# Kernel optimization log

Hardware: AMD Instinct MI355X
Metric: run time of the kernel (lower is better)

Reference implementation:

```python
import jax, jax.numpy as jnp
import numpy as np

N_VERTICES = 2000
N_SENSORY = 784
N_EDGES = 500_000
BATCH = 32
T_STEPS = 5
LR_VALUES = 0.1


def setup_inputs() -> dict:
    key = jax.random.key(0)
    k1, k2, k3 = jax.random.split(key, 3)
    values = jax.random.normal(k1, (BATCH, N_VERTICES), dtype=jnp.float32)
    # weight_init 'normal 0.0' -> std = max(0.01, 0) = 0.01 in the torch module
    weights = jax.random.normal(k2, (N_EDGES,), dtype=jnp.float32) * 0.01
    edge_index = jax.random.randint(k3, (2, N_EDGES), 0, N_VERTICES, dtype=jnp.int32)
    # sensory nodes (first 784) are clamped; only internal nodes update
    update_mask = jnp.arange(N_VERTICES) >= N_SENSORY  # bool [N]
    return {
        "values": values,
        "weights": weights,
        "edge_index": edge_index,
        "update_mask": update_mask,
        "T": T_STEPS,
    }


def reference(values, weights, edge_index, update_mask, T):
    """Iterative predictive-coding message passing.

    Each step:
      pred_i  = sum_{e: dst(e)=i} w_e * f(values[src(e)])   (gather-mul-scatter)
      err     = values - pred
      back_j  = sum_{e: src(e)=j} w_e * err[dst(e)]          (reverse scatter)
      dv      = err - f'(values) * back                      (dE/dx)
      values  = values - lr * dv   (sensory nodes clamped)
    """
    src, dst = edge_index[0], edge_index[1]
    n = values.shape[1]
    mask = update_mask[None, :]

    def step(v, _):
        fx = jnp.tanh(v)                                   # [B, N]
        msg = weights[None, :] * fx[:, src]                # [B, E]
        pred = jax.ops.segment_sum(msg.T, dst, num_segments=n).T  # [B, N]
        err = v - pred                                     # [B, N]
        w_err = weights[None, :] * err[:, dst]             # [B, E]
        back = jax.ops.segment_sum(w_err.T, src, num_segments=n).T  # [B, N]
        fprime = 1.0 - fx * fx                             # tanh'
        dv = err - fprime * back
        v_new = jnp.where(mask, v - LR_VALUES * dv, v)
        return v_new, None

    v_final, _ = jax.lax.scan(step, values, None, length=T)
    return v_final
```

## Files before the change

### kernel.cpp

```cpp
#include <hip/hip_runtime.h>
#include <hip/hip_bf16.h>


#define N_V     2000
#define N_SENS  784
#define N_INT   (N_V - N_SENS)
#define N_E     500000
#define T_STEPS 5
#define LR_VAL  0.1f
#define NVB     (N_V * 32)
#define NVH     (N_V * 16)
#define KP      2016
#define NCH     63
#define NT1     125
#define NT2     76
#define FRAG_N  (2 * NCH * 64 * 8)
#define NBLK    250
#define EPB     2000
#define NBLK_P  NT1
#define BAR_STRIDE 32

typedef float  f32x4 __attribute__((ext_vector_type(4)));
typedef short  s16x8 __attribute__((ext_vector_type(8)));
typedef unsigned long long u64;

__device__ __forceinline__ float bits_to_f32(unsigned u) {
    union { unsigned u; float f; } c; c.u = u; return c.f;
}
__device__ __forceinline__ unsigned f32_to_bits(float f) {
    union { float f; unsigned u; } c; c.f = f; return c.u;
}
__device__ __forceinline__ unsigned short f32_to_bf16(float f) {
    unsigned u = f32_to_bits(f);
    return (unsigned short)((u + 0x7FFFu + ((u >> 16) & 1u)) >> 16);
}
__device__ __forceinline__ float bf16_to_f32(unsigned short s) {
    return bits_to_f32((unsigned)s << 16);
}

__device__ __forceinline__ u64 ald64(const void* p) {
    return __hip_atomic_load((const u64*)p, __ATOMIC_RELAXED,
                             __HIP_MEMORY_SCOPE_AGENT);
}
__device__ __forceinline__ void ast64(void* p, u64 v) {
    __hip_atomic_store((u64*)p, v, __ATOMIC_RELAXED, __HIP_MEMORY_SCOPE_AGENT);
}
__device__ __forceinline__ unsigned short ald16(const unsigned short* p) {
    return __hip_atomic_load(p, __ATOMIC_RELAXED, __HIP_MEMORY_SCOPE_AGENT);
}
__device__ __forceinline__ void ast16(unsigned short* p, unsigned short v) {
    __hip_atomic_store(p, v, __ATOMIC_RELAXED, __HIP_MEMORY_SCOPE_AGENT);
}
__device__ __forceinline__ int cohld(const int* p) {
    int v;
    asm volatile("global_load_dword %0, %1, off sc0 sc1\n\ts_waitcnt vmcnt(0)"
                 : "=v"(v) : "v"(p) : "memory");
    return v;
}
__device__ __forceinline__ void cohst(int* p, int v) {
    asm volatile("global_store_dword %0, %1, off sc0 sc1"
                 :: "v"(p), "v"(v) : "memory");
}

__device__ __forceinline__ int aposKB(int k, int b) {
    int c = k >> 5, q = (k >> 3) & 3, j = k & 7;
    int h = b >> 4, m = b & 15;
    return (((h * NCH + c) * 64) + q * 16 + m) * 8 + j;
}


__global__ __launch_bounds__(256) void k_cnt(const int* __restrict__ dst,
                                             int* __restrict__ cnt_g,
                                             unsigned short* __restrict__ fxA,
                                             unsigned short* __restrict__ errA) {
    __shared__ int cnt[NT1];
    int b = blockIdx.x;
    {
        int t = b * 256 + threadIdx.x;
        if (t < 16 * 32) {
            int k = 2000 + (t >> 5), bb = t & 31;
            fxA[aposKB(k, bb)] = 0;
            errA[aposKB(k, bb)] = 0;
        }
    }
    for (int i = threadIdx.x; i < NT1; i += 256) cnt[i] = 0;
    __syncthreads();
    int base = b * EPB;
    for (int e = base + threadIdx.x; e < base + EPB; e += 256)
        atomicAdd(&cnt[dst[e] >> 4], 1);
    __syncthreads();
    for (int t = threadIdx.x; t < NT1; t += 256)
        cnt_g[t * 256 + b] = cnt[t];
}

__global__ __launch_bounds__(256) void k_scan_a(const int* __restrict__ cnt_g,
                                                int* __restrict__ base_g,
                                                int* __restrict__ totals) {
    __shared__ int sh[256];
    int t = blockIdx.x, tid = threadIdx.x;
    int v = (tid < NBLK) ? cnt_g[t * 256 + tid] : 0;
    sh[tid] = v;
    __syncthreads();
    for (int off = 1; off < 256; off <<= 1) {
        int x = (tid >= off) ? sh[tid - off] : 0;
        __syncthreads();
        sh[tid] += x;
        __syncthreads();
    }
    if (tid < NBLK) base_g[t * 256 + tid] = sh[tid] - v;
    if (tid == 255) totals[t] = sh[255];
}

__global__ void k_scan_b(const int* __restrict__ totals, int* __restrict__ tile_start) {
    if (threadIdx.x == 0 && blockIdx.x == 0) {
        int acc = 0;
        for (int t = 0; t < NT1; ++t) { tile_start[t] = acc; acc += totals[t]; }
        tile_start[NT1] = acc;
    }
}

__global__ __launch_bounds__(256) void k_place(
        const int* __restrict__ src, const int* __restrict__ dst,
        const float* __restrict__ w, const int* __restrict__ base_g,
        const int* __restrict__ tile_start, unsigned* __restrict__ pk_g) {
    __shared__ int cur[NT1];
    int b = blockIdx.x;
    for (int t = threadIdx.x; t < NT1; t += 256)
        cur[t] = tile_start[t] + base_g[t * 256 + b];
    __syncthreads();
    int base = b * EPB;
    for (int e = base + threadIdx.x; e < base + EPB; e += 256) {
        int d = dst[e];
        unsigned pk = ((unsigned)f32_to_bf16(w[e]) << 16)
                    | ((unsigned)(d & 15) << 11) | (unsigned)src[e];
        int p = atomicAdd(&cur[d >> 4], 1);
        pk_g[p] = pk;
    }
}

__global__ __launch_bounds__(256) void k_build(
        const unsigned* __restrict__ pk_g, const int* __restrict__ tile_start,
        uint4* __restrict__ WAbf4, unsigned short* __restrict__ WAd) {
    __shared__ float acc[8][KP];
    int tile = blockIdx.x >> 1, half = blockIdx.x & 1;
    for (int i = threadIdx.x; i < 8 * KP / 4; i += 256)
        ((float4*)&acc[0][0])[i] = make_float4(0.f, 0.f, 0.f, 0.f);
    __syncthreads();
    int beg = tile_start[tile], end = tile_start[tile + 1];
    for (int e = beg + threadIdx.x; e < end; e += 256) {
        unsigned pk = pk_g[e];
        int row = (int)((pk >> 11) & 15u);
        if ((row >> 3) == half)
            atomicAdd(&acc[row & 7][pk & 0x7FFu], bf16_to_f32((unsigned short)(pk >> 16)));
    }
    __syncthreads();
    for (int i = threadIdx.x; i < 8 * 252; i += 256) {
        int rr = i / 252, g = i - rr * 252;
        int c = g >> 2, q = g & 3;
        int col = g * 8;
        unsigned short r[8];
        #pragma unroll
        for (int j = 0; j < 8; ++j) r[j] = f32_to_bf16(acc[rr][col + j]);
        uint4 val = *(const uint4*)r;
        int m = half * 8 + rr;
        WAbf4[((tile * NCH + c) * 64) + q * 16 + m] = val;
        *(uint4*)(WAd + (size_t)(tile * 16 + m) * KP + col) = val;
    }
}

__global__ void k_trB(const unsigned short* __restrict__ WAd, uint4* __restrict__ WBf4) {
    int t = blockIdx.x * blockDim.x + threadIdx.x;
    if (t < NT2 * NCH * 64) {
        int tile = t / (NCH * 64);
        int rem = t - tile * (NCH * 64);
        int c = rem >> 6, l = rem & 63;
        int jcol = N_SENS + tile * 16 + (l & 15);
        int k0 = c * 32 + (l >> 4) * 8;
        unsigned short r[8];
        #pragma unroll
        for (int j = 0; j < 8; ++j)
            r[j] = (k0 + j < N_V) ? WAd[(size_t)(k0 + j) * KP + jcol] : (unsigned short)0;
        WBf4[t] = *(const uint4*)r;
    }
}

__global__ void k_init(const float* __restrict__ vin, float* __restrict__ v,
                       unsigned short* __restrict__ fxA, float* __restrict__ out,
                       int* __restrict__ bar) {
    int t = blockIdx.x * blockDim.x + threadIdx.x;
    if (t < (NBLK_P + 1) * BAR_STRIDE) bar[t] = 0;
    if (t < NVB) {
        float x = vin[t];
        int b = t / N_V;
        int i = t - b * N_V;
        v[(i << 5) + b] = x;
        fxA[aposKB(i, b)] = f32_to_bf16(tanhf(x));
        if (i < N_SENS) out[t] = x;
    }
}

__device__ __forceinline__ void gbar(int* arr, int epoch, int bx, int tid) {
    asm volatile("s_waitcnt vmcnt(0) lgkmcnt(0)" ::: "memory");
    __syncthreads();
    if (bx == 0) {
        if (tid == 0) cohst(&arr[0], epoch);
        if (tid < NBLK_P) {
            while (cohld(&arr[tid * BAR_STRIDE]) < epoch)
                __builtin_amdgcn_s_sleep(2);
        }
        __syncthreads();
        if (tid == 0) cohst(&arr[NBLK_P * BAR_STRIDE], epoch);
    } else {
        if (tid == 0) {
            cohst(&arr[bx * BAR_STRIDE], epoch);
            while (cohld(&arr[NBLK_P * BAR_STRIDE]) < epoch)
                __builtin_amdgcn_s_sleep(2);
        }
        __syncthreads();
    }
}

__global__ __launch_bounds__(512, 1) void k_loop(
        const uint4* __restrict__ WAbf4, const uint4* __restrict__ WBf4,
        unsigned short* fxA, unsigned short* errA,
        float* v_cur, float* __restrict__ out, int* arr) {
    __shared__ uint4 WldsA[NCH * 64];
    __shared__ uint4 WldsB[NCH * 64];
    __shared__ float red[2600];
    const int bx = blockIdx.x, tid = threadIdx.x;
    {
        const uint4* Wg = WAbf4 + (size_t)bx * (NCH * 64);
        for (int i = tid; i < NCH * 64; i += 512) WldsA[i] = Wg[i];
        if (bx < NT2) {
            const uint4* Wg2 = WBf4 + (size_t)bx * (NCH * 64);
            for (int i = tid; i < NCH * 64; i += 512) WldsB[i] = Wg2[i];
        }
    }
    const int w = tid >> 6, l = tid & 63;
    const int h = w >> 2, w4 = w & 3;
    const int cbeg = w4 * 16;
    float* my = &red[h * 1300 + w4 * 325 + l * 5];
    int epoch = 0;
    __syncthreads();

    for (int t = 0; t < T_STEPS; ++t) {
        {
            const u64* ap = (const u64*)fxA
                          + ((size_t)h * (NCH * 64) + cbeg * 64 + l) * 2;
            u64 f0[16], f1[16];
            #pragma unroll
            for (int cc = 0; cc < 16; ++cc)
                if (cbeg + cc < NCH) {
                    f0[cc] = ald64(ap + cc * 128);
                    f1[cc] = ald64(ap + cc * 128 + 1);
                }
            __builtin_amdgcn_sched_barrier(0);
            f32x4 acc = {0.f, 0.f, 0.f, 0.f};
            #pragma unroll
            for (int cc = 0; cc < 16; ++cc)
                if (cbeg + cc < NCH) {
                    u64 d[2] = {f0[cc], f1[cc]};
                    uint4 bfrag = WldsA[(cbeg + cc) * 64 + l];
                    acc = __builtin_amdgcn_mfma_f32_16x16x32_bf16(
                              *(s16x8*)d, *(s16x8*)&bfrag, acc, 0, 0, 0);
                }
            #pragma unroll
            for (int r = 0; r < 4; ++r) my[r] = acc[r];
            __syncthreads();
            if (w4 == 0) {
                float s[4];
                #pragma unroll
                for (int r = 0; r < 4; ++r)
                    s[r] = red[h * 1300 + l * 5 + r] + red[h * 1300 + 325 + l * 5 + r]
                         + red[h * 1300 + 650 + l * 5 + r] + red[h * 1300 + 975 + l * 5 + r];
                int i = bx * 16 + (l & 15);
                int q = l >> 4;
                int c2 = i >> 5, q2 = (i >> 3) & 3, j2 = i & 7;
                const float* vp = v_cur + (i << 5) + h * 16 + q * 4;
                union { u64 u[2]; float f[4]; } vu;
                vu.u[0] = ald64(vp);
                vu.u[1] = ald64(vp + 2);
                int base = ((h * NCH + c2) * 64 + q2 * 16) * 8 + j2;
                #pragma unroll
                for (int r = 0; r < 4; ++r)
                    ast16(&errA[base + (q * 4 + r) * 8],
                          f32_to_bf16(vu.f[r] - s[r]));
            }
        }
        ++epoch; gbar(arr, epoch, bx, tid);

        if (bx < NT2) {
            const u64* ap = (const u64*)errA
                          + ((size_t)h * (NCH * 64) + cbeg * 64 + l) * 2;
            u64 f0[16], f1[16];
            #pragma unroll
            for (int cc = 0; cc < 16; ++cc)
                if (cbeg + cc < NCH) {
                    f0[cc] = ald64(ap + cc * 128);
                    f1[cc] = ald64(ap + cc * 128 + 1);
                }
            __builtin_amdgcn_sched_barrier(0);
            f32x4 acc = {0.f, 0.f, 0.f, 0.f};
            #pragma unroll
            for (int cc = 0; cc < 16; ++cc)
                if (cbeg + cc < NCH) {
                    u64 d[2] = {f0[cc], f1[cc]};
                    uint4 bfrag = WldsB[(cbeg + cc) * 64 + l];
                    acc = __builtin_amdgcn_mfma_f32_16x16x32_bf16(
                              *(s16x8*)d, *(s16x8*)&bfrag, acc, 0, 0, 0);
                }
            #pragma unroll
            for (int r = 0; r < 4; ++r) my[r] = acc[r];
            __syncthreads();
            if (w4 == 0) {
                float s[4];
                #pragma unroll
                for (int r = 0; r < 4; ++r)
                    s[r] = red[h * 1300 + l * 5 + r] + red[h * 1300 + 325 + l * 5 + r]
                         + red[h * 1300 + 650 + l * 5 + r] + red[h * 1300 + 975 + l * 5 + r];
                int j = N_SENS + bx * 16 + (l & 15);
                int q = l >> 4;
                int c2 = j >> 5, q2 = (j >> 3) & 3, j2 = j & 7;
                float* vp = v_cur + (j << 5) + h * 16 + q * 4;
                union { u64 u[2]; float f[4]; } vu;
                vu.u[0] = ald64(vp);
                vu.u[1] = ald64(vp + 2);
                int base = ((h * NCH + c2) * 64 + q2 * 16) * 8 + j2;
                #pragma unroll
                for (int r = 0; r < 4; ++r) {
                    float e0 = bf16_to_f32(ald16(&errA[base + (q * 4 + r) * 8]));
                    float fxv = tanhf(vu.f[r]);
                    float vn = vu.f[r] - LR_VAL * (e0 - (1.f - fxv * fxv) * s[r]);
                    vu.f[r] = vn;
                    ast16(&fxA[base + (q * 4 + r) * 8], f32_to_bf16(tanhf(vn)));
                }
                ast64(vp, vu.u[0]);
                ast64(vp + 2, vu.u[1]);
                if (t == T_STEPS - 1) {
                    #pragma unroll
                    for (int r = 0; r < 4; ++r) {
                        int b = h * 16 + q * 4 + r;
                        out[b * N_V + j] = vu.f[r];
                    }
                }
            }
        }
        if (t < T_STEPS - 1) { ++epoch; gbar(arr, epoch, bx, tid); }
    }
}


__global__ void k_zero_i32(int* a, int n) {
    int t = blockIdx.x * blockDim.x + threadIdx.x;
    if (t < n) a[t] = 0;
}

__global__ void k_hist(const int* __restrict__ src, const int* __restrict__ dst,
                       int* cnt_dst, int* cnt_src) {
    int e = blockIdx.x * blockDim.x + threadIdx.x;
    if (e < N_E) {
        atomicAdd(&cnt_dst[dst[e]], 1);
        atomicAdd(&cnt_src[src[e]], 1);
    }
}

__global__ __launch_bounds__(1024) void k_scan(int* cnt_a, int* rp_a,
                                               int* cnt_b, int* rp_b) {
    __shared__ int sh[1024];
    int t = threadIdx.x;
    for (int pass = 0; pass < 2; ++pass) {
        int* cnt = pass ? cnt_b : cnt_a;
        int* rp  = pass ? rp_b  : rp_a;
        int i0 = 2 * t, i1 = 2 * t + 1;
        int c0 = (i0 < N_V) ? cnt[i0] : 0;
        int c1 = (i1 < N_V) ? cnt[i1] : 0;
        __syncthreads();
        sh[t] = c0 + c1;
        __syncthreads();
        for (int off = 1; off < 1024; off <<= 1) {
            int v = (t >= off) ? sh[t - off] : 0;
            __syncthreads();
            sh[t] += v;
            __syncthreads();
        }
        int incl = sh[t];
        int e0 = incl - (c0 + c1);
        int e1 = e0 + c0;
        if (i0 <= N_V) rp[i0] = e0;
        if (i1 <= N_V) rp[i1] = e1;
        if (i0 < N_V) cnt[i0] = e0;
        if (i1 < N_V) cnt[i1] = e1;
    }
}

__global__ void k_scatter(const int* __restrict__ src, const int* __restrict__ dst,
                          const float* __restrict__ w,
                          int* cur_dst, int* cur_src,
                          unsigned* __restrict__ pk_dst, unsigned* __restrict__ pk_src) {
    int e = blockIdx.x * blockDim.x + threadIdx.x;
    if (e < N_E) {
        int s = src[e], d = dst[e];
        unsigned wbits = (unsigned)f32_to_bf16(w[e]);
        int p = atomicAdd(&cur_dst[d], 1);
        pk_dst[p] = (wbits << 16) | (unsigned)s;
        int q = atomicAdd(&cur_src[s], 1);
        pk_src[q] = (wbits << 16) | (unsigned)d;
    }
}

__global__ void k_cast_in(const float* __restrict__ vin, float* __restrict__ v) {
    int t = blockIdx.x * blockDim.x + threadIdx.x;
    if (t < NVB) {
        int i = t >> 5, b = t & 31;
        v[t] = vin[b * N_V + i];
    }
}

__global__ void k_fx_csr(const float* __restrict__ v, unsigned short* __restrict__ fx) {
    int t = blockIdx.x * blockDim.x + threadIdx.x;
    if (t < NVB) {
        int i = t >> 5, b = t & 31;
        int h = b >> 4, b16 = b & 15;
        fx[h * NVH + i * 16 + b16] = f32_to_bf16(tanhf(v[t]));
    }
}

__global__ __launch_bounds__(256) void k_pred_err(
        const float* __restrict__ v, const unsigned short* __restrict__ fx,
        const int* __restrict__ rp, const unsigned* __restrict__ pk,
        unsigned short* __restrict__ err) {
    __shared__ unsigned short tab[NVH];
    int h  = blockIdx.x / 250;
    int vg = blockIdx.x % 250;
    {
        const uint4* g = (const uint4*)(fx + h * NVH);
        uint4* l = (uint4*)tab;
        for (int i = threadIdx.x; i < NVH / 8; i += 256) l[i] = g[i];
    }
    __syncthreads();
    int wave = threadIdx.x >> 6;
    int lane = threadIdx.x & 63;
    int b16 = lane & 15, epar = lane >> 4;
    for (int k = 0; k < 2; ++k) {
        int vid = vg * 8 + wave * 2 + k;
        int beg = rp[vid], end = rp[vid + 1];
        float sum = 0.f;
        for (int e = beg + epar; e < end; e += 4) {
            unsigned p = pk[e];
            float w = bits_to_f32(p & 0xFFFF0000u);
            int nb = (int)(p & 0xFFFFu);
            sum += w * bf16_to_f32(tab[nb * 16 + b16]);
        }
        sum += __shfl_xor(sum, 16, 64);
        sum += __shfl_xor(sum, 32, 64);
        if (epar == 0) {
            float vo = v[(vid << 5) + h * 16 + b16];
            err[h * NVH + vid * 16 + b16] = f32_to_bf16(vo - sum);
        }
    }
}

__global__ __launch_bounds__(256) void k_back_upd(
        const unsigned short* __restrict__ fx, const unsigned short* __restrict__ err,
        const int* __restrict__ rp, const unsigned* __restrict__ pk,
        float* __restrict__ v) {
    __shared__ unsigned short tab[NVH];
    int h  = blockIdx.x / 152;
    int vg = blockIdx.x % 152;
    {
        const uint4* g = (const uint4*)(err + h * NVH);
        uint4* l = (uint4*)tab;
        for (int i = threadIdx.x; i < NVH / 8; i += 256) l[i] = g[i];
    }
    __syncthreads();
    int wave = threadIdx.x >> 6;
    int lane = threadIdx.x & 63;
    int b16 = lane & 15, epar = lane >> 4;
    for (int k = 0; k < 2; ++k) {
        int vid = N_SENS + vg * 8 + wave * 2 + k;
        if (vid >= N_V) continue;
        int beg = rp[vid], end = rp[vid + 1];
        float sum = 0.f;
        for (int e = beg + epar; e < end; e += 4) {
            unsigned p = pk[e];
            float w = bits_to_f32(p & 0xFFFF0000u);
            int nb = (int)(p & 0xFFFFu);
            sum += w * bf16_to_f32(tab[nb * 16 + b16]);
        }
        sum += __shfl_xor(sum, 16, 64);
        sum += __shfl_xor(sum, 32, 64);
        if (epar == 0) {
            float e0  = bf16_to_f32(tab[vid * 16 + b16]);
            float fxv = bf16_to_f32(fx[h * NVH + vid * 16 + b16]);
            float dv = e0 - (1.f - fxv * fxv) * sum;
            v[(vid << 5) + h * 16 + b16] -= LR_VAL * dv;
        }
    }
}

__global__ void k_out_fb(const float* __restrict__ v, float* __restrict__ out) {
    int t = blockIdx.x * blockDim.x + threadIdx.x;
    if (t < NVB) {
        int b = t / N_V;
        int i = t - b * N_V;
        out[t] = v[(i << 5) + b];
    }
}


extern "C" void kernel_launch(void* const* d_in, const int* in_sizes, int n_in,
                              void* d_out, int out_size, void* d_ws, size_t ws_size,
                              hipStream_t stream) {
    const float* vals = (const float*)d_in[0];
    const float* wts  = (const float*)d_in[1];
    const int* ei = (const int*)d_in[2];
    const int* src = ei;
    const int* dst = ei + N_E;
    float* out = (float*)d_out;

    const int EB = (N_E + 255) / 256;

    const size_t WABF_T = (size_t)NT1 * NCH * 64;
    const size_t WBF_T  = (size_t)NT2 * NCH * 64;
    const size_t WAD_N  = (size_t)N_V * KP;
    const size_t need = (size_t)N_E * 4 + 2 * NT1 * 256 * 4 + 512 * 4
                      + WAD_N * 2 + WABF_T * 16 + WBF_T * 16
                      + 2 * (size_t)FRAG_N * 2 + NVB * 4 + 256;

    if (ws_size >= need) {
        unsigned* pk_g = (unsigned*)d_ws;
        int* cnt_g  = (int*)(pk_g + N_E);
        int* base_g = cnt_g + NT1 * 256;
        int* totals = base_g + NT1 * 256;
        int* tile_start = totals + 128;
        unsigned short* WAd = (unsigned short*)(tile_start + 384);
        uint4* WAbf4 = (uint4*)(WAd + WAD_N);
        uint4* WBf4  = WAbf4 + WABF_T;
        unsigned short* fxA  = (unsigned short*)(WBf4 + WBF_T);
        unsigned short* errA = fxA + FRAG_N;
        float* v_cur = (float*)(errA + FRAG_N);
        int* bar_arr = (int*)pk_g;

        k_cnt<<<NBLK, 256, 0, stream>>>(dst, cnt_g, fxA, errA);
        k_scan_a<<<NT1, 256, 0, stream>>>(cnt_g, base_g, totals);
        k_scan_b<<<1, 64, 0, stream>>>(totals, tile_start);
        k_place<<<NBLK, 256, 0, stream>>>(src, dst, wts, base_g, tile_start, pk_g);
        k_build<<<2 * NT1, 256, 0, stream>>>(pk_g, tile_start, WAbf4, WAd);
        k_trB<<<(int)((WBF_T + 255) / 256), 256, 0, stream>>>(WAd, WBf4);
        k_init<<<250, 256, 0, stream>>>(vals, v_cur, fxA, out, bar_arr);

        k_loop<<<NBLK_P, 512, 0, stream>>>(WAbf4, WBf4, fxA, errA, v_cur, out,
                                           bar_arr);
    } else {
        float* v_cur = (float*)d_ws;
        unsigned short* fx_g  = (unsigned short*)(v_cur + NVB);
        unsigned short* err_g = fx_g + NVB;
        int* rp_dst  = (int*)(err_g + NVB);
        int* rp_src  = rp_dst + 2048;
        int* cur_dst = rp_src + 2048;
        int* cur_src = cur_dst + 2048;
        unsigned* pk_dst = (unsigned*)(cur_src + 2048);
        unsigned* pk_src = pk_dst + N_E;

        k_zero_i32<<<16, 256, 0, stream>>>(cur_dst, 4096);
        k_hist<<<EB, 256, 0, stream>>>(src, dst, cur_dst, cur_src);
        k_scan<<<1, 1024, 0, stream>>>(cur_dst, rp_dst, cur_src, rp_src);
        k_scatter<<<EB, 256, 0, stream>>>(src, dst, wts, cur_dst, cur_src,
                                          pk_dst, pk_src);
        k_cast_in<<<250, 256, 0, stream>>>(vals, v_cur);
        for (int t = 0; t < T_STEPS; ++t) {
            k_fx_csr<<<250, 256, 0, stream>>>(v_cur, fx_g);
            k_pred_err<<<500, 256, 0, stream>>>(v_cur, fx_g, rp_dst, pk_dst, err_g);
            k_back_upd<<<304, 256, 0, stream>>>(fx_g, err_g, rp_src, pk_src, v_cur);
        }
        k_out_fb<<<250, 256, 0, stream>>>(v_cur, out);
    }
}
```

Baseline: 159.5 us.

## Fold scan, transpose and init kernels into neighbors to cut launches

Removes k_scan_b, k_trB and k_init. The prefix sum of tile totals is recomputed inside k_place and k_build, and the value/tanh init plus barrier zeroing move into k_cnt. k_build now handles all 16 rows per tile in one block and writes a transposed internal-row matrix, which k_loop reads directly to fill its B-operand LDS tile instead of reading a pre-built fragment buffer. This cuts the pipeline from eight launches to five. In exchange, k_build uses twice the shared memory per block with half as many blocks, and each block repeats a serial 125-element scan.

Result: faster. 153.6 us (-3.7%).

```diff
diff --git a/kernel.cpp b/kernel.cpp
--- a/kernel.cpp
+++ b/kernel.cpp
@@ -19,6 +19,7 @@
 #define EPB     2000
 #define NBLK_P  NT1
 #define BAR_STRIDE 32
+#define BAR_N   ((NBLK_P + 1) * BAR_STRIDE)
 
 typedef float  f32x4 __attribute__((ext_vector_type(4)));
 typedef short  s16x8 __attribute__((ext_vector_type(8)));
@@ -72,16 +73,34 @@
 __global__ __launch_bounds__(256) void k_cnt(const int* __restrict__ dst,
                                              int* __restrict__ cnt_g,
                                              unsigned short* __restrict__ fxA,
-                                             unsigned short* __restrict__ errA) {
+                                             unsigned short* __restrict__ errA,
+                                             const float* __restrict__ vin,
+                                             float* __restrict__ v,
+                                             float* __restrict__ out,
+                                             unsigned short* __restrict__ WAdT,
+                                             int* __restrict__ bar) {
     __shared__ int cnt[NT1];
     int b = blockIdx.x;
+    int t = b * 256 + threadIdx.x;
     {
-        int t = b * 256 + threadIdx.x;
         if (t < 16 * 32) {
             int k = 2000 + (t >> 5), bb = t & 31;
             fxA[aposKB(k, bb)] = 0;
             errA[aposKB(k, bb)] = 0;
         }
+        if (t < N_INT * 2) {
+            uint4 z = {0u, 0u, 0u, 0u};
+            *(uint4*)(WAdT + (size_t)(t >> 1) * KP + 2000 + (t & 1) * 8) = z;
+        }
+        if (t < BAR_N) bar[t] = 0;
+    }
+    if (t < NVB) {
+        float x = vin[t];
+        int bb = t / N_V;
+        int i = t - bb * N_V;
+        v[(i << 5) + bb] = x;
+        fxA[aposKB(i, bb)] = f32_to_bf16(tanhf(x));
+        if (i < N_SENS) out[t] = x;
     }
     for (int i = threadIdx.x; i < NT1; i += 256) cnt[i] = 0;
     __syncthreads();
@@ -89,8 +108,8 @@
     for (int e = base + threadIdx.x; e < base + EPB; e += 256)
         atomicAdd(&cnt[dst[e] >> 4], 1);
     __syncthreads();
-    for (int t = threadIdx.x; t < NT1; t += 256)
-        cnt_g[t * 256 + b] = cnt[t];
+    for (int tt = threadIdx.x; tt < NT1; tt += 256)
+        cnt_g[tt * 256 + b] = cnt[tt];
 }
 
 __global__ __launch_bounds__(256) void k_scan_a(const int* __restrict__ cnt_g,
@@ -111,22 +130,20 @@
     if (tid == 255) totals[t] = sh[255];
 }
 
-__global__ void k_scan_b(const int* __restrict__ totals, int* __restrict__ tile_start) {
-    if (threadIdx.x == 0 && blockIdx.x == 0) {
-        int acc = 0;
-        for (int t = 0; t < NT1; ++t) { tile_start[t] = acc; acc += totals[t]; }
-        tile_start[NT1] = acc;
-    }
-}
-
 __global__ __launch_bounds__(256) void k_place(
         const int* __restrict__ src, const int* __restrict__ dst,
         const float* __restrict__ w, const int* __restrict__ base_g,
-        const int* __restrict__ tile_start, unsigned* __restrict__ pk_g) {
+        const int* __restrict__ totals, unsigned* __restrict__ pk_g) {
     __shared__ int cur[NT1];
+    __shared__ int ts[NT1];
     int b = blockIdx.x;
+    if (threadIdx.x == 0) {
+        int a = 0;
+        for (int t = 0; t < NT1; ++t) { ts[t] = a; a += totals[t]; }
+    }
+    __syncthreads();
     for (int t = threadIdx.x; t < NT1; t += 256)
-        cur[t] = tile_start[t] + base_g[t * 256 + b];
+        cur[t] = ts[t] + base_g[t * 256 + b];
     __syncthreads();
     int base = b * EPB;
     for (int e = base + threadIdx.x; e < base + EPB; e += 256) {
@@ -139,63 +156,43 @@
 }
 
 __global__ __launch_bounds__(256) void k_build(
-        const unsigned* __restrict__ pk_g, const int* __restrict__ tile_start,
-        uint4* __restrict__ WAbf4, unsigned short* __restrict__ WAd) {
-    __shared__ float acc[8][KP];
-    int tile = blockIdx.x >> 1, half = blockIdx.x & 1;
-    for (int i = threadIdx.x; i < 8 * KP / 4; i += 256)
+        const unsigned* __restrict__ pk_g, const int* __restrict__ totals,
+        uint4* __restrict__ WAbf4, unsigned short* __restrict__ WAdT) {
+    __shared__ float acc[16][KP];
+    __shared__ int ts[NT1 + 1];
+    int tile = blockIdx.x;
+    for (int i = threadIdx.x; i < 16 * KP / 4; i += 256)
         ((float4*)&acc[0][0])[i] = make_float4(0.f, 0.f, 0.f, 0.f);
-    __syncthreads();
-    int beg = tile_start[tile], end = tile_start[tile + 1];
+    if (threadIdx.x == 0) {
+        int a = 0;
+        for (int t = 0; t < NT1; ++t) { ts[t] = a; a += totals[t]; }
+        ts[NT1] = a;
+    }
+    __syncthreads();
+    int beg = ts[tile], end = ts[tile + 1];
     for (int e = beg + threadIdx.x; e < end; e += 256) {
         unsigned pk = pk_g[e];
         int row = (int)((pk >> 11) & 15u);
-        if ((row >> 3) == half)
-            atomicAdd(&acc[row & 7][pk & 0x7FFu], bf16_to_f32((unsigned short)(pk >> 16)));
-    }
-    __syncthreads();
-    for (int i = threadIdx.x; i < 8 * 252; i += 256) {
-        int rr = i / 252, g = i - rr * 252;
+        atomicAdd(&acc[row][pk & 0x7FFu], bf16_to_f32((unsigned short)(pk >> 16)));
+    }
+    __syncthreads();
+    for (int i = threadIdx.x; i < 16 * 252; i += 256) {
+        int m = i / 252, g = i - m * 252;
         int c = g >> 2, q = g & 3;
         int col = g * 8;
         unsigned short r[8];
         #pragma unroll
-        for (int j = 0; j < 8; ++j) r[j] = f32_to_bf16(acc[rr][col + j]);
-        uint4 val = *(const uint4*)r;
-        int m = half * 8 + rr;
-        WAbf4[((tile * NCH + c) * 64) + q * 16 + m] = val;
-        *(uint4*)(WAd + (size_t)(tile * 16 + m) * KP + col) = val;
-    }
-}
-
-__global__ void k_trB(const unsigned short* __restrict__ WAd, uint4* __restrict__ WBf4) {
-    int t = blockIdx.x * blockDim.x + threadIdx.x;
-    if (t < NT2 * NCH * 64) {
-        int tile = t / (NCH * 64);
-        int rem = t - tile * (NCH * 64);
-        int c = rem >> 6, l = rem & 63;
-        int jcol = N_SENS + tile * 16 + (l & 15);
-        int k0 = c * 32 + (l >> 4) * 8;
-        unsigned short r[8];
+        for (int j = 0; j < 8; ++j) r[j] = f32_to_bf16(acc[m][col + j]);
+        WAbf4[((tile * NCH + c) * 64) + q * 16 + m] = *(const uint4*)r;
+    }
+    for (int i = threadIdx.x; i < N_INT; i += 256) {
+        int j = N_SENS + i;
+        unsigned short r[16];
         #pragma unroll
-        for (int j = 0; j < 8; ++j)
-            r[j] = (k0 + j < N_V) ? WAd[(size_t)(k0 + j) * KP + jcol] : (unsigned short)0;
-        WBf4[t] = *(const uint4*)r;
-    }
-}
-
-__global__ void k_init(const float* __restrict__ vin, float* __restrict__ v,
-                       unsigned short* __restrict__ fxA, float* __restrict__ out,
-                       int* __restrict__ bar) {
-    int t = blockIdx.x * blockDim.x + threadIdx.x;
-    if (t < (NBLK_P + 1) * BAR_STRIDE) bar[t] = 0;
-    if (t < NVB) {
-        float x = vin[t];
-        int b = t / N_V;
-        int i = t - b * N_V;
-        v[(i << 5) + b] = x;
-        fxA[aposKB(i, b)] = f32_to_bf16(tanhf(x));
-        if (i < N_SENS) out[t] = x;
+        for (int m = 0; m < 16; ++m) r[m] = f32_to_bf16(acc[m][j]);
+        uint4* p = (uint4*)(WAdT + (size_t)i * KP + tile * 16);
+        p[0] = *(const uint4*)r;
+        p[1] = *(const uint4*)(r + 8);
     }
 }
 
@@ -221,7 +218,7 @@
 }
 
 __global__ __launch_bounds__(512, 1) void k_loop(
-        const uint4* __restrict__ WAbf4, const uint4* __restrict__ WBf4,
+        const uint4* __restrict__ WAbf4, const unsigned short* __restrict__ WAdT,
         unsigned short* fxA, unsigned short* errA,
         float* v_cur, float* __restrict__ out, int* arr) {
     __shared__ uint4 WldsA[NCH * 64];
@@ -232,8 +229,12 @@
         const uint4* Wg = WAbf4 + (size_t)bx * (NCH * 64);
         for (int i = tid; i < NCH * 64; i += 512) WldsA[i] = Wg[i];
         if (bx < NT2) {
-            const uint4* Wg2 = WBf4 + (size_t)bx * (NCH * 64);
-            for (int i = tid; i < NCH * 64; i += 512) WldsB[i] = Wg2[i];
+            for (int i = tid; i < NCH * 64; i += 512) {
+                int c = i >> 6, ll = i & 63;
+                int row = bx * 16 + (ll & 15);
+                int k0 = c * 32 + (ll >> 4) * 8;
+                WldsB[i] = *(const uint4*)(WAdT + (size_t)row * KP + k0);
+            }
         }
     }
     const int w = tid >> 6, l = tid & 63;
@@ -521,35 +522,30 @@
     const int EB = (N_E + 255) / 256;
 
     const size_t WABF_T = (size_t)NT1 * NCH * 64;
-    const size_t WBF_T  = (size_t)NT2 * NCH * 64;
-    const size_t WAD_N  = (size_t)N_V * KP;
-    const size_t need = (size_t)N_E * 4 + 2 * NT1 * 256 * 4 + 512 * 4
-                      + WAD_N * 2 + WABF_T * 16 + WBF_T * 16
-                      + 2 * (size_t)FRAG_N * 2 + NVB * 4 + 256;
+    const size_t WADT_N = (size_t)N_INT * KP;
+    const size_t need = (size_t)N_E * 4 + 2 * NT1 * 256 * 4 + 512
+                      + WADT_N * 2 + WABF_T * 16
+                      + 2 * (size_t)FRAG_N * 2 + NVB * 4
+                      + (size_t)BAR_N * 4 + 256;
 
     if (ws_size >= need) {
         unsigned* pk_g = (unsigned*)d_ws;
         int* cnt_g  = (int*)(pk_g + N_E);
         int* base_g = cnt_g + NT1 * 256;
         int* totals = base_g + NT1 * 256;
-        int* tile_start = totals + 128;
-        unsigned short* WAd = (unsigned short*)(tile_start + 384);
-        uint4* WAbf4 = (uint4*)(WAd + WAD_N);
-        uint4* WBf4  = WAbf4 + WABF_T;
-        unsigned short* fxA  = (unsigned short*)(WBf4 + WBF_T);
+        unsigned short* WAdT = (unsigned short*)(totals + 128);
+        uint4* WAbf4 = (uint4*)(WAdT + WADT_N);
+        unsigned short* fxA  = (unsigned short*)(WAbf4 + WABF_T);
         unsigned short* errA = fxA + FRAG_N;
         float* v_cur = (float*)(errA + FRAG_N);
-        int* bar_arr = (int*)pk_g;
-
-        k_cnt<<<NBLK, 256, 0, stream>>>(dst, cnt_g, fxA, errA);
+        int* bar_arr = (int*)(v_cur + NVB);
+
+        k_cnt<<<NBLK, 256, 0, stream>>>(dst, cnt_g, fxA, errA, vals, v_cur,
+                                        out, WAdT, bar_arr);
         k_scan_a<<<NT1, 256, 0, stream>>>(cnt_g, base_g, totals);
-        k_scan_b<<<1, 64, 0, stream>>>(totals, tile_start);
-        k_place<<<NBLK, 256, 0, stream>>>(src, dst, wts, base_g, tile_start, pk_g);
-        k_build<<<2 * NT1, 256, 0, stream>>>(pk_g, tile_start, WAbf4, WAd);
-        k_trB<<<(int)((WBF_T + 255) / 256), 256, 0, stream>>>(WAd, WBf4);
-        k_init<<<250, 256, 0, stream>>>(vals, v_cur, fxA, out, bar_arr);
-
-        k_loop<<<NBLK_P, 512, 0, stream>>>(WAbf4, WBf4, fxA, errA, v_cur, out,
+        k_place<<<NBLK, 256, 0, stream>>>(src, dst, wts, base_g, totals, pk_g);
+        k_build<<<NT1, 256, 0, stream>>>(pk_g, totals, WAbf4, WAdT);
+        k_loop<<<NBLK_P, 512, 0, stream>>>(WAbf4, WAdT, fxA, errA, v_cur, out,
                                            bar_arr);
     } else {
         float* v_cur = (float*)d_ws;
```
